# Kernel tuning notes

Measured on AMD Instinct MI355X. Metric: run time of the kernel, lower is better.

## Reference

```python
import jax, jax.numpy as jnp
import numpy as np

B = 4096        # number of (drug, disease) pair graphs
N_PER = 60      # nodes per subgraph (>= k)
N = B * N_PER   # 245760 total nodes
E = 2_000_000   # edges
F_IN = 64
L1, L2 = 32, 32 # latent_dim
K = 30          # sort-pool k
N_DRUG, N_DIS = 1024, 2048


def gcn_conv(x, src, dst, W, b, n):
    # PyG GCNConv (eval): h = XW; symmetric norm with self-loops; out = A_hat h + b
    h = x @ W
    deg = jax.ops.segment_sum(jnp.ones(src.shape[0], h.dtype), dst, num_segments=n) + 1.0
    dinv = deg ** -0.5
    msg = h[src] * (dinv[src] * dinv[dst])[:, None]
    out = jax.ops.segment_sum(msg, dst, num_segments=n)
    out = out + h * (dinv * dinv)[:, None]  # self-loop contribution
    return out + b


def dense_gcn(x, adj, W, b):
    # PyG DenseGCNConv: set diag to 1, D^-1/2 A D^-1/2, out = A_hat (x W) + b
    n = adj.shape[0]
    eye = jnp.eye(n, dtype=adj.dtype)
    a = adj * (1.0 - eye) + eye
    deg = a.sum(-1)
    dinv = jnp.where(deg > 0, deg ** -0.5, 0.0)
    a = dinv[:, None] * a * dinv[None, :]
    return a @ (x @ W) + b


def conv1d(x, w, b, stride):
    out = jax.lax.conv_general_dilated(x, w, (stride,), 'VALID',
                                       dimension_numbers=('NCH', 'OIH', 'NCH'))
    return out + b[None, :, None]


def setup_inputs():
    key = jax.random.key(0)
    ks = jax.random.split(key, 24)
    x = jax.random.normal(ks[0], (N, F_IN), jnp.float32)
    edge_index = jax.random.randint(ks[1], (2, E), 0, N)
    batch = jnp.repeat(jnp.arange(B), N_PER)
    node = jnp.stack([jax.random.randint(ks[2], (B,), 0, N_DRUG),
                      jax.random.randint(ks[3], (B,), 0, N_DIS)], axis=1)
    di_sim = jax.random.normal(ks[4], (N_DRUG, N_DRUG), jnp.float32)
    dr_sim = jax.random.normal(ks[5], (N_DIS, N_DIS), jnp.float32)
    drug_adj = jax.random.uniform(ks[6], (N_DRUG, N_DRUG), jnp.float32)
    dis_adj = jax.random.uniform(ks[7], (N_DIS, N_DIS), jnp.float32)
    p = jnp.array(0.5, jnp.float32)

    def w(k, shape):
        return jax.random.normal(k, shape, jnp.float32) * 0.05

    z = lambda s: jnp.zeros(s, jnp.float32)
    params = dict(
        W1=w(ks[8], (F_IN, L1)), b1=z((L1,)),
        W2=w(ks[9], (L1, L2)), b2=z((L2,)),
        W3=w(ks[10], (256, 64)), b3=z((64,)),
        W4=w(ks[11], (64, 16)), b4=z((16,)),
        lin_di_w=w(ks[12], (N_DRUG, 256)), lin_di_b=z((256,)),
        lin_dr_w=w(ks[13], (N_DIS, 256)), lin_dr_b=z((256,)),
        c1_w=w(ks[14], (128, 1, L1 + L2)), c1_b=z((128,)),
        c2_w=w(ks[15], (256, 128, 5)), c2_b=z((256,)),
        lin1_w=w(ks[16], (2816, 128)), lin1_b=z((128,)),
        lin2_w=w(ks[17], (128, 32)), lin2_b=z((32,)),
        bn_g=jnp.ones((32,), jnp.float32), bn_b=z((32,)),
        fcs_w=w(ks[18], (64, 32)), fcs_b=z((32,)),
        fcs2_w=w(ks[19], (32, 1)), fcs2_b=z((1,)),
    )
    return dict(x=x, edge_index=edge_index, batch=batch, node=node,
                di_sim=di_sim, dr_sim=dr_sim, drug_adj=drug_adj,
                dis_adj=dis_adj, p=p, **params)


def reference(x, edge_index, batch, node, di_sim, dr_sim, drug_adj, dis_adj, p,
              W1, b1, W2, b2, W3, b3, W4, b4,
              lin_di_w, lin_di_b, lin_dr_w, lin_dr_b,
              c1_w, c1_b, c2_w, c2_b, lin1_w, lin1_b, lin2_w, lin2_b,
              bn_g, bn_b, fcs_w, fcs_b, fcs2_w, fcs2_b):
    src, dst = edge_index[0], edge_index[1]
    # two GCN layers over the pair subgraphs
    x1 = jax.nn.relu(gcn_conv(x, src, dst, W1, b1, N))
    x2 = jax.nn.relu(gcn_conv(x1, src, dst, W2, b2, N))
    cs = jnp.concatenate([x1, x2], axis=1)       # [N, 64]
    D = cs.shape[1]
    # sort-pool: equal-size graphs, batch contiguous -> reshape and sort per graph
    xb = cs.reshape(B, N_PER, D)
    order = jnp.argsort(-xb[:, :, -1], axis=-1)  # descending by last channel
    xs = jnp.take_along_axis(xb, order[:, :, None], axis=1)[:, :K]  # [B, K, D]
    h = xs.reshape(B, 1, K * D)
    h = jax.nn.relu(conv1d(h, c1_w, c1_b, D))    # [B, 128, K]
    h = jax.lax.reduce_window(h, -jnp.inf, jax.lax.max, (1, 1, 2), (1, 1, 2), 'VALID')
    h = jax.nn.relu(conv1d(h, c2_w, c2_b, 1))    # [B, 256, 11]
    h = h.reshape(B, -1)                         # [B, 2816]
    h = jax.nn.relu(h @ lin1_w + lin1_b)
    h = h @ lin2_w + lin2_b
    h = jax.nn.relu(h * bn_g + bn_b)             # BatchNorm eval (mean 0, var 1)
    # dense similarity-graph branches (conv3/conv4 weights shared across branches)
    di_e = di_sim @ lin_di_w + lin_di_b
    di_f = jax.nn.relu(dense_gcn(di_e, drug_adj, W3, b3))
    di_o = jax.nn.relu(dense_gcn(di_f, drug_adj, W4, b4))
    di = di_o[node[:, 0]]
    dr_e = dr_sim @ lin_dr_w + lin_dr_b
    dr_f = jax.nn.relu(dense_gcn(dr_e, dis_adj, W3, b3))
    dr_o = jax.nn.relu(dense_gcn(dr_f, dis_adj, W4, b4))
    dr = dr_o[node[:, 1]]
    feat = jnp.concatenate([di, dr], axis=1)     # [B, 32]
    z = jnp.concatenate([h * p, feat * (1.0 - p)], axis=1)  # [B, 64]
    z = jax.nn.relu(z @ fcs_w + fcs_b)
    return (z @ fcs2_w + fcs2_b)[:, 0]
```

## Files before the change

kernel.cpp:

```cpp
#include <hip/hip_runtime.h>

#define NN 245760
#define NB 4096
#define NPER 60
#define NE 2000000
#define KSEL 30
#define NDRUG 1024
#define NDIS 2048
#define NBKT 480
#define CHUNK 8192
#define SEGCAP 4992

typedef unsigned short ushort_t;
typedef unsigned int uint_t;
using bf16x8 = __attribute__((ext_vector_type(8))) short;
using f32x4 = __attribute__((ext_vector_type(4))) float;

__device__ inline ushort_t f2bf(float f) {
    union { float f; unsigned int u; } v; v.f = f;
    unsigned int r = v.u + 0x7FFF + ((v.u >> 16) & 1);
    return (ushort_t)(r >> 16);
}

__global__ void k_bcount(const int* __restrict__ ei, int* __restrict__ bcnt) {
    __shared__ int h[NBKT];
    int t = threadIdx.x;
    for (int i = t; i < NBKT; i += 256) h[i] = 0;
    __syncthreads();
    for (int e = blockIdx.x * 256 + t; e < NE; e += gridDim.x * 256)
        atomicAdd(&h[ei[NE + e] >> 9], 1);
    __syncthreads();
    for (int i = t; i < NBKT; i += 256) if (h[i]) atomicAdd(&bcnt[i], h[i]);
}

__global__ void k_bscan(const int* __restrict__ bcnt, int* __restrict__ bofs) {
    __shared__ int a[512], b_[512];
    int t = threadIdx.x;
    int v = (t < NBKT) ? bcnt[t] : 0;
    a[t] = v; __syncthreads();
    int* src = a; int* dst = b_;
    for (int off = 1; off < 512; off <<= 1) {
        dst[t] = src[t] + ((t >= off) ? src[t - off] : 0);
        __syncthreads();
        int* tmp = src; src = dst; dst = tmp;
    }
    if (t < NBKT) bofs[t] = src[t] - v;
}

__global__ __launch_bounds__(256) void k_bscatter(const int* __restrict__ ei,
                                                  const int* __restrict__ bofs,
                                                  int* __restrict__ bfill,
                                                  uint_t* __restrict__ pairs) {
    __shared__ int hist[NBKT], fill[NBKT], gbase[NBKT];
    int t = threadIdx.x;
    long e0 = (long)blockIdx.x * CHUNK;
    int cnt = (int)min((long)CHUNK, (long)NE - e0);
    for (int i = t; i < NBKT; i += 256) { hist[i] = 0; fill[i] = 0; }
    __syncthreads();
    for (int i = t; i < cnt; i += 256)
        atomicAdd(&hist[ei[NE + e0 + i] >> 9], 1);
    __syncthreads();
    for (int i = t; i < NBKT; i += 256)
        if (hist[i]) gbase[i] = bofs[i] + atomicAdd(&bfill[i], hist[i]);
    __syncthreads();
    for (int i = t; i < cnt; i += 256) {
        int s = ei[e0 + i], d = ei[NE + e0 + i];
        int b = d >> 9;
        int pos = gbase[b] + atomicAdd(&fill[b], 1);
        pairs[pos] = ((uint_t)s << 9) | (uint_t)(d & 511);
    }
}

__global__ __launch_bounds__(256) void k_bbuild(const uint_t* __restrict__ pairs,
                                                const int* __restrict__ bofs,
                                                const int* __restrict__ bcnt,
                                                int* __restrict__ csr,
                                                int* __restrict__ rowp,
                                                int* __restrict__ cntg,
                                                float* __restrict__ dinv) {
    __shared__ int hist[512], nbase[512], nfill[512], scanA[512], scanB[512];
    __shared__ int seg[SEGCAP];
    int t = threadIdx.x, b = blockIdx.x;
    int ebase = bofs[b], ecnt = bcnt[b];
    if (ecnt > SEGCAP) ecnt = SEGCAP;
    for (int i = t; i < 512; i += 256) { hist[i] = 0; nfill[i] = 0; }
    __syncthreads();
    for (int i = t; i < ecnt; i += 256)
        atomicAdd(&hist[pairs[ebase + i] & 511], 1);
    __syncthreads();
    for (int i = t; i < 512; i += 256) scanA[i] = hist[i];
    __syncthreads();
    int* src = scanA; int* dst = scanB;
    for (int off = 1; off < 512; off <<= 1) {
        for (int i = t; i < 512; i += 256)
            dst[i] = src[i] + ((i >= off) ? src[i - off] : 0);
        __syncthreads();
        int* tmp = src; src = dst; dst = tmp;
    }
    for (int i = t; i < 512; i += 256) {
        int h = hist[i];
        int excl = src[i] - h;
        nbase[i] = excl;
        int n = (b << 9) + i;
        rowp[n] = ebase + excl;
        cntg[n] = h;
        dinv[n] = 1.0f / sqrtf((float)h + 1.0f);
    }
    __syncthreads();
    for (int i = t; i < ecnt; i += 256) {
        uint_t v = pairs[ebase + i];
        int ln = v & 511;
        int pos = nbase[ln] + atomicAdd(&nfill[ln], 1);
        if (pos < SEGCAP) seg[pos] = (int)(v >> 9);
    }
    __syncthreads();
    for (int i = t; i < ecnt; i += 256) csr[ebase + i] = seg[i];
}

__global__ __launch_bounds__(256) void k_xw(const float* __restrict__ A, const float* __restrict__ W,
                                            float* __restrict__ h, int K, int lda) {
    __shared__ float Xs[64][65];
    __shared__ float Ws[64][32];
    int t = threadIdx.x;
    int r0 = blockIdx.x * 64;
    int kq = K >> 2;
    for (int idx = t; idx < 64 * kq; idx += 256) {
        int row = idx / kq, q = idx % kq;
        float4 v = *(const float4*)(A + (long)(r0 + row) * lda + q * 4);
        Xs[row][q * 4 + 0] = v.x; Xs[row][q * 4 + 1] = v.y;
        Xs[row][q * 4 + 2] = v.z; Xs[row][q * 4 + 3] = v.w;
    }
    for (int idx = t; idx < K * 32; idx += 256) ((float*)Ws)[idx] = W[idx];
    __syncthreads();
    int r = (t >> 3) * 2, c = (t & 7) * 4;
    float4 acc0 = {0, 0, 0, 0}, acc1 = {0, 0, 0, 0};
    for (int k = 0; k < K; k++) {
        float x0 = Xs[r][k], x1 = Xs[r + 1][k];
        float4 w = *(const float4*)&Ws[k][c];
        acc0.x += x0 * w.x; acc0.y += x0 * w.y; acc0.z += x0 * w.z; acc0.w += x0 * w.w;
        acc1.x += x1 * w.x; acc1.y += x1 * w.y; acc1.z += x1 * w.z; acc1.w += x1 * w.w;
    }
    *(float4*)(h + (long)(r0 + r) * 32 + c) = acc0;
    *(float4*)(h + (long)(r0 + r + 1) * 32 + c) = acc1;
}

__global__ void k_gcn_agg(const float* __restrict__ h, const int* __restrict__ csr,
                          const int* __restrict__ rowp, const int* __restrict__ cnt,
                          const float* __restrict__ dinv, const float* __restrict__ bias,
                          float* __restrict__ out, int colofs) {
    int t = threadIdx.x;
    int l = t & 7, g = t >> 3;
    int wl = t & 63;
    int gbase = wl & ~7;
    int d = blockIdx.x * 32 + g;
    float dd = dinv[d];
    int start = rowp[d], c = cnt[d];
    float4 hv = *(const float4*)(h + (long)d * 32 + l * 4);
    float4 acc; acc.x = dd * hv.x; acc.y = dd * hv.y; acc.z = dd * hv.z; acc.w = dd * hv.w;
    int k = 0;
    while (k < c) {
        int nb = c - k; if (nb > 8) nb = 8;
        int sl = (l < nb) ? csr[start + k + l] : 0;
        int sj[8]; float ds[8]; float4 hj[8];
#pragma unroll
        for (int j = 0; j < 8; j++)
            sj[j] = __shfl(sl, gbase + j, 64);
#pragma unroll
        for (int j = 0; j < 8; j++)
            if (j < nb) ds[j] = dinv[sj[j]];
#pragma unroll
        for (int j = 0; j < 8; j++)
            if (j < nb) hj[j] = *(const float4*)(h + (long)sj[j] * 32 + l * 4);
#pragma unroll
        for (int j = 0; j < 8; j++) {
            if (j < nb) {
                acc.x += ds[j] * hj[j].x;
                acc.y += ds[j] * hj[j].y;
                acc.z += ds[j] * hj[j].z;
                acc.w += ds[j] * hj[j].w;
            }
        }
        k += nb;
    }
    float4 bv = *(const float4*)(bias + l * 4);
    float* op = out + (long)d * 64 + colofs + l * 4;
    op[0] = fmaxf(dd * acc.x + bv.x, 0.f);
    op[1] = fmaxf(dd * acc.y + bv.y, 0.f);
    op[2] = fmaxf(dd * acc.z + bv.z, 0.f);
    op[3] = fmaxf(dd * acc.w + bv.w, 0.f);
}

__global__ __launch_bounds__(256, 2) void k_conv1_mfma(const float* __restrict__ cs,
                                                       const int* __restrict__ sel,
                                                       const ushort_t* __restrict__ c1w16,
                                                       const float* __restrict__ c1b,
                                                       ushort_t* __restrict__ po16) {
    __shared__ ushort_t A_lds[128 * 72];
    __shared__ ushort_t B_lds[128 * 72];
    int t = threadIdx.x;
    int r0 = blockIdx.x * 128;
#pragma unroll
    for (int rnd = 0; rnd < 4; rnd++) {
        int idx = t + rnd * 256;
        int row = idx >> 3, seg = idx & 7;
        const float* src = cs + (long)sel[r0 + row] * 64 + seg * 8;
        float4 v0 = *(const float4*)src;
        float4 v1 = *(const float4*)(src + 4);
        ushort_t tmp[8] = {f2bf(v0.x), f2bf(v0.y), f2bf(v0.z), f2bf(v0.w),
                           f2bf(v1.x), f2bf(v1.y), f2bf(v1.z), f2bf(v1.w)};
        *(uint4*)&A_lds[row * 72 + seg * 8] = *(uint4*)tmp;
        *(uint4*)&B_lds[row * 72 + seg * 8] = *(const uint4*)(c1w16 + row * 64 + seg * 8);
    }
    __syncthreads();
    int wv = t >> 6, lane = t & 63;
    int wm = wv >> 1, wn = wv & 1;
    int lrow = lane & 15, lk = (lane >> 4) * 8, lr4 = (lane >> 4) * 4;
    f32x4 acc[4][4] = {};
#pragma unroll
    for (int kk = 0; kk < 2; kk++) {
        bf16x8 a[4], b[4];
#pragma unroll
        for (int f = 0; f < 4; f++) {
            a[f] = *(const bf16x8*)&A_lds[(wm * 64 + f * 16 + lrow) * 72 + kk * 32 + lk];
            b[f] = *(const bf16x8*)&B_lds[(wn * 64 + f * 16 + lrow) * 72 + kk * 32 + lk];
        }
#pragma unroll
        for (int i = 0; i < 4; i++)
#pragma unroll
            for (int j = 0; j < 4; j++)
                acc[i][j] = __builtin_amdgcn_mfma_f32_16x16x32_bf16(a[i], b[j], acc[i][j], 0, 0, 0);
    }
    __syncthreads();
    ushort_t* po_lds = A_lds;
#pragma unroll
    for (int fn = 0; fn < 4; fn++) {
        int col = wn * 64 + fn * 16 + lrow;
        float bb = c1b[col];
#pragma unroll
        for (int fm = 0; fm < 4; fm++) {
            int lrow2 = wm * 32 + fm * 8 + (lr4 >> 1);
            float v0 = fmaxf(acc[fm][fn][0] + bb, 0.f);
            float v1 = fmaxf(acc[fm][fn][1] + bb, 0.f);
            float v2 = fmaxf(acc[fm][fn][2] + bb, 0.f);
            float v3 = fmaxf(acc[fm][fn][3] + bb, 0.f);
            po_lds[lrow2 * 128 + col]       = f2bf(fmaxf(v0, v1));
            po_lds[(lrow2 + 1) * 128 + col] = f2bf(fmaxf(v2, v3));
        }
    }
    __syncthreads();
    uint4* dst = (uint4*)(po16 + (long)(r0 >> 1) * 128);
    const uint4* srcp = (const uint4*)po_lds;
#pragma unroll
    for (int i = 0; i < 4; i++) dst[t + i * 256] = srcp[t + i * 256];
}

__global__ __launch_bounds__(256, 2) void k_conv2_mfma(const ushort_t* __restrict__ pool16,
                                                       const ushort_t* __restrict__ w2colT,
                                                       ushort_t* __restrict__ act2,
                                                       const float* __restrict__ bias) {
    __shared__ ushort_t smem[2 * 128 * 72];
    ushort_t* A_lds = smem;
    ushort_t* B_lds = smem + 128 * 72;
    int t = threadIdx.x;
    int r0 = blockIdx.x * 128, c0 = blockIdx.y * 128;
    long abase[4]; const ushort_t* bptr[4]; int lofs[4];
#pragma unroll
    for (int rnd = 0; rnd < 4; rnd++) {
        int idx = t + rnd * 256;
        int row = idx >> 3, seg = idx & 7;
        int arow = r0 + row;
        int bb = arow / 11, tt2 = arow - bb * 11;
        abase[rnd] = (long)(bb * 15 + tt2) * 128 + seg * 8;
        bptr[rnd] = w2colT + (long)(c0 + row) * 640 + seg * 8;
        lofs[rnd] = row * 72 + seg * 8;
    }
    int wv = t >> 6, lane = t & 63;
    int wm = wv >> 1, wn = wv & 1;
    int lrow = lane & 15, lk = (lane >> 4) * 8, lr4 = (lane >> 4) * 4;
    f32x4 acc[4][4] = {};
    for (int k0 = 0; k0 < 640; k0 += 64) {
#pragma unroll
        for (int rnd = 0; rnd < 4; rnd++) {
            *(uint4*)&A_lds[lofs[rnd]] = *(const uint4*)(pool16 + abase[rnd] + k0);
            *(uint4*)&B_lds[lofs[rnd]] = *(const uint4*)(bptr[rnd] + k0);
        }
        __syncthreads();
#pragma unroll
        for (int kk = 0; kk < 2; kk++) {
            bf16x8 a[4], b[4];
#pragma unroll
            for (int f = 0; f < 4; f++) {
                a[f] = *(const bf16x8*)&A_lds[(wm * 64 + f * 16 + lrow) * 72 + kk * 32 + lk];
                b[f] = *(const bf16x8*)&B_lds[(wn * 64 + f * 16 + lrow) * 72 + kk * 32 + lk];
            }
#pragma unroll
            for (int i = 0; i < 4; i++)
#pragma unroll
                for (int j = 0; j < 4; j++)
                    acc[i][j] = __builtin_amdgcn_mfma_f32_16x16x32_bf16(a[i], b[j], acc[i][j], 0, 0, 0);
        }
        __syncthreads();
    }
    ushort_t* c_lds = smem;
#pragma unroll
    for (int fn = 0; fn < 4; fn++) {
        int col = wn * 64 + fn * 16 + lrow;
        float bv = bias[c0 + col];
#pragma unroll
        for (int fm = 0; fm < 4; fm++) {
            int lr = wm * 64 + fm * 16 + lr4;
#pragma unroll
            for (int j = 0; j < 4; j++)
                c_lds[(lr + j) * 128 + col] = f2bf(fmaxf(acc[fm][fn][j] + bv, 0.f));
        }
    }
    __syncthreads();
#pragma unroll
    for (int i = 0; i < 8; i++) {
        int idx = t + i * 256;
        int row = idx >> 4, q = idx & 15;
        *(uint4*)(act2 + (long)(r0 + row) * 256 + c0 + q * 8) = ((const uint4*)c_lds)[idx];
    }
}

__global__ __launch_bounds__(256, 2) void k_lin1_mfma(const ushort_t* __restrict__ A,
                                                      const ushort_t* __restrict__ Bm,
                                                      float* __restrict__ C) {
    __shared__ ushort_t A_lds[128 * 72];
    __shared__ ushort_t B_lds[128 * 72];
    int t = threadIdx.x;
    int r0 = blockIdx.x * 128;
    int kz = blockIdx.z;
    const ushort_t* ap[4]; const ushort_t* bp[4]; int lofs[4];
#pragma unroll
    for (int rnd = 0; rnd < 4; rnd++) {
        int idx = t + rnd * 256;
        int row = idx >> 3, seg = idx & 7;
        ap[rnd] = A + (long)(r0 + row) * 2816 + kz * 704 + seg * 8;
        bp[rnd] = Bm + (long)row * 2816 + kz * 704 + seg * 8;
        lofs[rnd] = row * 72 + seg * 8;
    }
    int wv = t >> 6, lane = t & 63;
    int wm = wv >> 1, wn = wv & 1;
    int lrow = lane & 15, lk = (lane >> 4) * 8, lr4 = (lane >> 4) * 4;
    f32x4 acc[4][4] = {};
    for (int k0 = 0; k0 < 704; k0 += 64) {
#pragma unroll
        for (int rnd = 0; rnd < 4; rnd++) {
            *(uint4*)&A_lds[lofs[rnd]] = *(const uint4*)(ap[rnd] + k0);
            *(uint4*)&B_lds[lofs[rnd]] = *(const uint4*)(bp[rnd] + k0);
        }
        __syncthreads();
#pragma unroll
        for (int kk = 0; kk < 2; kk++) {
            bf16x8 a[4], b[4];
#pragma unroll
            for (int f = 0; f < 4; f++) {
                a[f] = *(const bf16x8*)&A_lds[(wm * 64 + f * 16 + lrow) * 72 + kk * 32 + lk];
                b[f] = *(const bf16x8*)&B_lds[(wn * 64 + f * 16 + lrow) * 72 + kk * 32 + lk];
            }
#pragma unroll
            for (int i = 0; i < 4; i++)
#pragma unroll
                for (int j = 0; j < 4; j++)
                    acc[i][j] = __builtin_amdgcn_mfma_f32_16x16x32_bf16(a[i], b[j], acc[i][j], 0, 0, 0);
        }
        __syncthreads();
    }
#pragma unroll
    for (int fn = 0; fn < 4; fn++) {
        int col = wn * 64 + fn * 16 + lrow;
#pragma unroll
        for (int fm = 0; fm < 4; fm++) {
            int rowb = r0 + wm * 64 + fm * 16 + lr4;
#pragma unroll
            for (int j = 0; j < 4; j++)
                atomicAdd(&C[(long)(rowb + j) * 128 + col], acc[fm][fn][j]);
        }
    }
}

__global__ __launch_bounds__(256, 2) void k_de_mfma(
    const ushort_t* __restrict__ A0, const ushort_t* __restrict__ B0, float* __restrict__ C0,
    const float* __restrict__ bias0, int M0, int K0, int KS0,
    const ushort_t* __restrict__ A1, const ushort_t* __restrict__ B1, float* __restrict__ C1,
    const float* __restrict__ bias1, int M1, int K1, int KS1) {
    __shared__ ushort_t A_lds[128 * 72];
    __shared__ ushort_t B_lds[64 * 72];
    int z = blockIdx.z;
    const ushort_t* A; const ushort_t* Bm; float* C; const float* bias; int M, K, kz, KS;
    if (z < KS0) { A = A0; Bm = B0; C = C0; bias = bias0; M = M0; K = K0; kz = z; KS = KS0; }
    else { A = A1; Bm = B1; C = C1; bias = bias1; M = M1; K = K1; kz = z - KS0; KS = KS1; }
    int r0 = blockIdx.x * 128, c0 = blockIdx.y * 64;
    if (r0 >= M) return;
    int Kc = K / KS;
    int kb = kz * Kc;
    int t = threadIdx.x;
    const ushort_t* ap[4]; int alofs[4];
#pragma unroll
    for (int rnd = 0; rnd < 4; rnd++) {
        int idx = t + rnd * 256;
        int row = idx >> 3, seg = idx & 7;
        ap[rnd] = A + (long)(r0 + row) * K + kb + seg * 8;
        alofs[rnd] = row * 72 + seg * 8;
    }
    const ushort_t* bp[2]; int blofs[2];
#pragma unroll
    for (int rnd = 0; rnd < 2; rnd++) {
        int idx = t + rnd * 256;
        int row = idx >> 3, seg = idx & 7;
        bp[rnd] = Bm + (long)(c0 + row) * K + kb + seg * 8;
        blofs[rnd] = row * 72 + seg * 8;
    }
    int wv = t >> 6, lane = t & 63;
    int lrow = lane & 15, lk = (lane >> 4) * 8, lr4 = (lane >> 4) * 4;
    uint4 areg[4], breg[2];
#pragma unroll
    for (int rnd = 0; rnd < 4; rnd++) areg[rnd] = *(const uint4*)(ap[rnd]);
#pragma unroll
    for (int rnd = 0; rnd < 2; rnd++) breg[rnd] = *(const uint4*)(bp[rnd]);
    f32x4 acc[2][4] = {};
    for (int k0 = 0; k0 < Kc; k0 += 64) {
#pragma unroll
        for (int rnd = 0; rnd < 4; rnd++) *(uint4*)&A_lds[alofs[rnd]] = areg[rnd];
#pragma unroll
        for (int rnd = 0; rnd < 2; rnd++) *(uint4*)&B_lds[blofs[rnd]] = breg[rnd];
        __syncthreads();
        if (k0 + 64 < Kc) {
#pragma unroll
            for (int rnd = 0; rnd < 4; rnd++) areg[rnd] = *(const uint4*)(ap[rnd] + k0 + 64);
#pragma unroll
            for (int rnd = 0; rnd < 2; rnd++) breg[rnd] = *(const uint4*)(bp[rnd] + k0 + 64);
        }
#pragma unroll
        for (int kk = 0; kk < 2; kk++) {
            bf16x8 a[2], b[4];
#pragma unroll
            for (int f = 0; f < 2; f++)
                a[f] = *(const bf16x8*)&A_lds[(wv * 32 + f * 16 + lrow) * 72 + kk * 32 + lk];
#pragma unroll
            for (int f = 0; f < 4; f++)
                b[f] = *(const bf16x8*)&B_lds[(f * 16 + lrow) * 72 + kk * 32 + lk];
#pragma unroll
            for (int i = 0; i < 2; i++)
#pragma unroll
                for (int j = 0; j < 4; j++)
                    acc[i][j] = __builtin_amdgcn_mfma_f32_16x16x32_bf16(a[i], b[j], acc[i][j], 0, 0, 0);
        }
        __syncthreads();
    }
#pragma unroll
    for (int fn = 0; fn < 4; fn++) {
        int col = c0 + fn * 16 + lrow;
        float bv = (kz == 0) ? bias[col] : 0.f;
#pragma unroll
        for (int fm = 0; fm < 2; fm++) {
            int rowb = r0 + wv * 32 + fm * 16 + lr4;
#pragma unroll
            for (int j = 0; j < 4; j++)
                atomicAdd(&C[(long)(rowb + j) * 256 + col], acc[fm][fn][j] + bv);
        }
    }
}

__global__ __launch_bounds__(256, 2) void k_g_mfma(
    const ushort_t* __restrict__ A0, const ushort_t* __restrict__ B0, float* __restrict__ C0,
    int M0, int K0, int KS0,
    const ushort_t* __restrict__ A1, const ushort_t* __restrict__ B1, float* __restrict__ C1,
    int M1, int K1, int KS1) {
    __shared__ ushort_t A_lds[128 * 72];
    __shared__ ushort_t B_lds[64 * 72];
    int z = blockIdx.z;
    const ushort_t* A; const ushort_t* Bm; float* C; int M, K, kz, KS;
    if (z < KS0) { A = A0; Bm = B0; C = C0; M = M0; K = K0; kz = z; KS = KS0; }
    else { A = A1; Bm = B1; C = C1; M = M1; K = K1; kz = z - KS0; KS = KS1; }
    int r0 = blockIdx.x * 128;
    if (r0 >= M) return;
    int Kc = K / KS;
    int kb = kz * Kc;
    int t = threadIdx.x;
    const ushort_t* ap[4]; int alofs[4];
#pragma unroll
    for (int rnd = 0; rnd < 4; rnd++) {
        int idx = t + rnd * 256;
        int row = idx >> 3, seg = idx & 7;
        ap[rnd] = A + (long)(r0 + row) * K + kb + seg * 8;
        alofs[rnd] = row * 72 + seg * 8;
    }
    const ushort_t* bp[2]; int blofs[2];
#pragma unroll
    for (int rnd = 0; rnd < 2; rnd++) {
        int idx = t + rnd * 256;
        int row = idx >> 3, seg = idx & 7;
        bp[rnd] = Bm + (long)row * K + kb + seg * 8;
        blofs[rnd] = row * 72 + seg * 8;
    }
    int wv = t >> 6, lane = t & 63;
    int lrow = lane & 15, lk = (lane >> 4) * 8, lr4 = (lane >> 4) * 4;
    uint4 areg[4], breg[2];
#pragma unroll
    for (int rnd = 0; rnd < 4; rnd++) areg[rnd] = *(const uint4*)(ap[rnd]);
#pragma unroll
    for (int rnd = 0; rnd < 2; rnd++) breg[rnd] = *(const uint4*)(bp[rnd]);
    f32x4 acc[2][4] = {};
    for (int k0 = 0; k0 < Kc; k0 += 64) {
#pragma unroll
        for (int rnd = 0; rnd < 4; rnd++) *(uint4*)&A_lds[alofs[rnd]] = areg[rnd];
#pragma unroll
        for (int rnd = 0; rnd < 2; rnd++) *(uint4*)&B_lds[blofs[rnd]] = breg[rnd];
        __syncthreads();
        if (k0 + 64 < Kc) {
#pragma unroll
            for (int rnd = 0; rnd < 4; rnd++) areg[rnd] = *(const uint4*)(ap[rnd] + k0 + 64);
#pragma unroll
            for (int rnd = 0; rnd < 2; rnd++) breg[rnd] = *(const uint4*)(bp[rnd] + k0 + 64);
        }
#pragma unroll
        for (int kk = 0; kk < 2; kk++) {
            bf16x8 a[2], b[4];
#pragma unroll
            for (int f = 0; f < 2; f++)
                a[f] = *(const bf16x8*)&A_lds[(wv * 32 + f * 16 + lrow) * 72 + kk * 32 + lk];
#pragma unroll
            for (int f = 0; f < 4; f++)
                b[f] = *(const bf16x8*)&B_lds[(f * 16 + lrow) * 72 + kk * 32 + lk];
#pragma unroll
            for (int i = 0; i < 2; i++)
#pragma unroll
                for (int j = 0; j < 4; j++)
                    acc[i][j] = __builtin_amdgcn_mfma_f32_16x16x32_bf16(a[i], b[j], acc[i][j], 0, 0, 0);
        }
        __syncthreads();
    }
#pragma unroll
    for (int fn = 0; fn < 4; fn++) {
        int col = fn * 16 + lrow;
#pragma unroll
        for (int fm = 0; fm < 2; fm++) {
            int rowb = r0 + wv * 32 + fm * 16 + lr4;
#pragma unroll
            for (int j = 0; j < 4; j++)
                atomicAdd(&C[(long)(rowb + j) * 64 + col], acc[fm][fn][j]);
        }
    }
}

__global__ void k_cvt2(const float* __restrict__ a0, ushort_t* __restrict__ o0, long n0,
                       const float* __restrict__ a1, ushort_t* __restrict__ o1, long n1) {
    long i4 = ((long)blockIdx.x * 256 + threadIdx.x) * 4;
    const float* a; ushort_t* o;
    if (i4 < n0) { a = a0 + i4; o = o0 + i4; }
    else {
        long j = i4 - n0;
        if (j >= n1) return;
        a = a1 + j; o = o1 + j;
    }
    float4 v = *(const float4*)a;
    o[0] = f2bf(v.x); o[1] = f2bf(v.y); o[2] = f2bf(v.z); o[3] = f2bf(v.w);
}

__global__ void k_linwT2(const float* __restrict__ w0, ushort_t* __restrict__ o0, int K0,
                         const float* __restrict__ w1, ushort_t* __restrict__ o1, int K1) {
    __shared__ float tile[64][65];
    int nb0 = K0 / 64;
    int bx = blockIdx.x;
    const float* w; ushort_t* o; int K, kt;
    if (bx < nb0) { w = w0; o = o0; K = K0; kt = bx; }
    else { w = w1; o = o1; K = K1; kt = bx - nb0; }
    int n0 = blockIdx.y * 64, k0 = kt * 64;
    int t = threadIdx.x;
    int r = t >> 6, c = t & 63;
    for (int rr = r; rr < 64; rr += 4)
        tile[rr][c] = w[(long)(k0 + rr) * 256 + n0 + c];
    __syncthreads();
    for (int rr = r; rr < 64; rr += 4)
        o[(long)(n0 + rr) * K + k0 + c] = f2bf(tile[c][rr]);
}

__global__ void k_uT2(const float* __restrict__ u0, ushort_t* __restrict__ o0, int K0,
                      const float* __restrict__ u1, ushort_t* __restrict__ o1, int K1) {
    __shared__ float tile[64][65];
    int nb0 = K0 / 64;
    int bx = blockIdx.x;
    const float* u; ushort_t* o; int K, kt;
    if (bx < nb0) { u = u0; o = o0; K = K0; kt = bx; }
    else { u = u1; o = o1; K = K1; kt = bx - nb0; }
    int k0 = kt * 64;
    int t = threadIdx.x;
    int r = t >> 6, c = t & 63;
    for (int rr = r; rr < 64; rr += 4)
        tile[rr][c] = u[(long)(k0 + rr) * 64 + c];
    __syncthreads();
    for (int rr = r; rr < 64; rr += 4)
        o[(long)rr * K + k0 + c] = f2bf(tile[c][rr]);
}

__global__ __launch_bounds__(256) void k_gemm_sk(
    const float* A0, const float* B0, float* C0, const float* ab0p, const float* cs0p,
    int M0, int N0, int K0, int lda0, int KS0, int Kc0,
    const float* A1, const float* B1, float* C1, const float* ab1p, const float* cs1p,
    int M1, int N1, int K1, int lda1, int KS1, int Kc1) {
    int z = blockIdx.z;
    const float* A; const float* Bm; float* C; const float* abp; const float* csp;
    int M, N, K, lda, kz, Kc;
    if (z < KS0) { A = A0; Bm = B0; C = C0; abp = ab0p; csp = cs0p; M = M0; N = N0; K = K0; lda = lda0; kz = z; Kc = Kc0; }
    else { A = A1; Bm = B1; C = C1; abp = ab1p; csp = cs1p; M = M1; N = N1; K = K1; lda = lda1; kz = z - KS0; Kc = Kc1; }
    int r0 = blockIdx.x * 64, c0 = blockIdx.y * 64;
    if (r0 >= M || c0 >= N) return;
    int kb = kz * Kc, ke = min(K, kb + Kc);
    __shared__ float As[16][68];
    __shared__ float Bs[16][68];
    int t = threadIdx.x;
    int tx = t & 15, ty = t >> 4;
    float acc[4][4] = {};
    int ar = t >> 2, aq = (t & 3) * 4;
    long abase = (long)(r0 + ar) * lda;
    int brow = t >> 4, bc = (t & 15) * 4;
    float4 av = *(const float4*)(A + abase + kb + aq);
    if (abp) {
        float4 abv = *(const float4*)(abp + kb + aq);
        av.x += abv.x; av.y += abv.y; av.z += abv.z; av.w += abv.w;
    }
    float4 bv = *(const float4*)(Bm + (long)(kb + brow) * N + c0 + bc);
    for (int k0 = kb; k0 < ke; k0 += 16) {
        As[aq + 0][ar] = av.x; As[aq + 1][ar] = av.y; As[aq + 2][ar] = av.z; As[aq + 3][ar] = av.w;
        *(float4*)&Bs[brow][bc] = bv;
        __syncthreads();
        if (k0 + 16 < ke) {
            av = *(const float4*)(A + abase + k0 + 16 + aq);
            if (abp) {
                float4 abv = *(const float4*)(abp + k0 + 16 + aq);
                av.x += abv.x; av.y += abv.y; av.z += abv.z; av.w += abv.w;
            }
            bv = *(const float4*)(Bm + (long)(k0 + 16 + brow) * N + c0 + bc);
        }
#pragma unroll
        for (int kk = 0; kk < 16; kk++) {
            float4 a4 = *(const float4*)&As[kk][ty * 4];
            float4 b4 = *(const float4*)&Bs[kk][tx * 4];
            float aa[4] = {a4.x, a4.y, a4.z, a4.w};
            float bb2[4] = {b4.x, b4.y, b4.z, b4.w};
#pragma unroll
            for (int i = 0; i < 4; i++)
#pragma unroll
                for (int j = 0; j < 4; j++) acc[i][j] += aa[i] * bb2[j];
        }
        __syncthreads();
    }
#pragma unroll
    for (int i = 0; i < 4; i++) {
        int row = r0 + ty * 4 + i;
        float sc = csp ? csp[row] : 1.0f;
#pragma unroll
        for (int j = 0; j < 4; j++)
            atomicAdd(&C[(long)row * N + c0 + tx * 4 + j], acc[i][j] * sc);
    }
}

__global__ void k_dense_deg2(const float* __restrict__ adj0, float* __restrict__ d0, int n0,
                             const float* __restrict__ adj1, float* __restrict__ d1, int n1) {
    int lane = threadIdx.x & 63;
    int row = (blockIdx.x * blockDim.x + threadIdx.x) >> 6;
    const float* adj; float* dv; int n, r;
    if (row < n0) { adj = adj0; dv = d0; n = n0; r = row; }
    else {
        r = row - n0;
        if (r >= n1) return;
        adj = adj1; dv = d1; n = n1;
    }
    const float* rp = adj + (long)r * n;
    float s = 0.f;
    for (int j = lane; j < n; j += 64) s += rp[j];
    for (int off = 32; off > 0; off >>= 1) s += __shfl_down(s, off, 64);
    if (lane == 0) {
        float deg = s - rp[r] + 1.0f;
        dv[r] = (deg > 0.f) ? 1.0f / sqrtf(deg) : 0.f;
    }
}

__global__ void k_fix_w4(const float* g0, const float* u0, const float* adj0, const float* d0, float* o0, int n0,
                         const float* g1, const float* u1, const float* adj1, const float* d1, float* o1, int n1,
                         const float* __restrict__ b3, const float* __restrict__ W4) {
    __shared__ float dfs[16][68];
    __shared__ float W4s[64 * 16];
    int t = threadIdx.x;
    for (int i = t; i < 1024; i += 256) W4s[i] = W4[i];
    int bx = blockIdx.x, nb0 = n0 / 16;
    const float* g; const float* u; const float* adj; const float* dv; float* o; int n, r0;
    if (bx < nb0) { g = g0; u = u0; adj = adj0; dv = d0; o = o0; n = n0; r0 = bx * 16; }
    else { g = g1; u = u1; adj = adj1; dv = d1; o = o1; n = n1; r0 = (bx - nb0) * 16; }
    int r = t >> 4;
    int row = r0 + r;
    float di = dv[row];
    float om = 1.0f - adj[(long)row * n + row];
    int c4 = (t & 15) * 4;
    float4 gv = *(const float4*)(g + (long)row * 64 + c4);
    float4 uv = *(const float4*)(u + (long)row * 64 + c4);
    float4 bv = *(const float4*)(b3 + c4);
    dfs[r][c4 + 0] = fmaxf(di * (gv.x + om * uv.x) + bv.x, 0.f);
    dfs[r][c4 + 1] = fmaxf(di * (gv.y + om * uv.y) + bv.y, 0.f);
    dfs[r][c4 + 2] = fmaxf(di * (gv.z + om * uv.z) + bv.z, 0.f);
    dfs[r][c4 + 3] = fmaxf(di * (gv.w + om * uv.w) + bv.w, 0.f);
    __syncthreads();
    int c = t & 15;
    float accv = 0.f;
#pragma unroll
    for (int k = 0; k < 64; k++) accv += dfs[r][k] * W4s[k * 16 + c];
    o[row * 16 + c] = di * accv;
}

__global__ void k_fixup2(const float* g0, const float* t0, const float* adj0, const float* d0, float* C0, long n0,
                         const float* g1, const float* t1, const float* adj1, const float* d1, float* C1, long n1,
                         const float* bias, int cols) {
    long idx = (long)blockIdx.x * 256 + threadIdx.x;
    long s0 = n0 * cols;
    const float* g; const float* tt; const float* adj; const float* dv; float* C; long n, li;
    if (idx < s0) { g = g0; tt = t0; adj = adj0; dv = d0; C = C0; n = n0; li = idx; }
    else {
        li = idx - s0;
        if (li >= n1 * cols) return;
        g = g1; tt = t1; adj = adj1; dv = d1; C = C1; n = n1;
    }
    long i = li / cols; int j = li % cols;
    float v = dv[i] * (g[li] + (1.0f - adj[i * n + i]) * tt[li]) + bias[j];
    C[li] = fmaxf(v, 0.f);
}

__global__ void k_adj16(const float* adj0, const float* u0, float* C0, int n0, int KS0, int Kc0,
                        const float* adj1, const float* u1, float* C1, int n1, int KS1, int Kc1) {
    int z = blockIdx.z;
    const float* adj; const float* u; float* C; int n, kz, Kc;
    if (z < KS0) { adj = adj0; u = u0; C = C0; n = n0; kz = z; Kc = Kc0; }
    else { adj = adj1; u = u1; C = C1; n = n1; kz = z - KS0; Kc = Kc1; }
    int r0 = blockIdx.x * 16;
    if (r0 >= n) return;
    int t = threadIdx.x;
    int r = r0 + (t >> 4), c = t & 15;
    int kb = kz * Kc, ke = min(n, kb + Kc);
    const float* arp = adj + (long)r * n;
    float acc = 0.f;
    for (int k = kb; k < ke; k += 4) {
        float4 a = *(const float4*)(arp + k);
        acc += a.x * u[(k + 0) * 16 + c] + a.y * u[(k + 1) * 16 + c]
             + a.z * u[(k + 2) * 16 + c] + a.w * u[(k + 3) * 16 + c];
    }
    atomicAdd(&C[r * 16 + c], acc);
}

__global__ void k_select(const float* __restrict__ cs, int* __restrict__ sel) {
    __shared__ float kk[240];
    int t = threadIdx.x;
    int b0 = blockIdx.x * 4;
    if (t < 240) kk[t] = cs[((long)(b0 * 60 + t)) * 64 + 63];
    __syncthreads();
    if (t < 240) {
        int lb = t / 60, i = t % 60;
        float key = kk[lb * 60 + i];
        int r = 0;
        for (int j = 0; j < 60; j++) {
            float kj = kk[lb * 60 + j];
            r += (kj > key) || (kj == key && j < i);
        }
        if (r < KSEL) sel[(b0 + lb) * KSEL + r] = (b0 + lb) * 60 + i;
    }
}

__global__ void k_w2colT(const float* __restrict__ c2w, ushort_t* __restrict__ o) {
    int idx = blockIdx.x * blockDim.x + threadIdx.x;
    if (idx >= 256 * 640) return;
    int oc = idx / 640, q = idx % 640;
    int tap = q >> 7, ic = q & 127;
    o[idx] = f2bf(c2w[(oc * 128 + ic) * 5 + tap]);
}

__global__ void k_w1pT(const float* __restrict__ w, ushort_t* __restrict__ o) {
    int idx = blockIdx.x * blockDim.x + threadIdx.x;
    if (idx >= 128 * 2816) return;
    int j = idx / 2816, c = idx % 2816;
    int tt = c >> 8, oc = c & 255;
    o[idx] = f2bf(w[(oc * 11 + tt) * 128 + j]);
}

__global__ void k_lin2_bn(const float* __restrict__ x, const float* __restrict__ l1b,
                          const float* __restrict__ w,
                          const float* __restrict__ b, const float* __restrict__ g,
                          const float* __restrict__ bb, float* __restrict__ o) {
    int t = blockIdx.x * blockDim.x + threadIdx.x;
    int j = t & 31, bi = t >> 5;
    const float* xr = x + (long)bi * 128;
    float acc = b[j];
    for (int k = 0; k < 128; k++) acc += fmaxf(xr[k] + l1b[k], 0.f) * w[k * 32 + j];
    o[bi * 32 + j] = fmaxf(acc * g[j] + bb[j], 0.f);
}

__global__ __launch_bounds__(256) void k_final(const float* __restrict__ hfin, const int* __restrict__ node,
                                               const float* __restrict__ dio, const float* __restrict__ dro,
                                               const float* __restrict__ pp,
                                               const float* __restrict__ fw, const float* __restrict__ fb,
                                               const float* __restrict__ f2w, const float* __restrict__ f2b,
                                               float* __restrict__ out) {
    __shared__ float w[64 * 32];
    __shared__ float w2[32];
    int t = threadIdx.x;
    for (int f = t; f < 2048; f += 256) w[f] = fw[f];
    if (t < 32) w2[t] = f2w[t];
    __syncthreads();
    int b = blockIdx.x * 256 + t;
    float p = *pp, q = 1.0f - p;
    float zin[64];
#pragma unroll
    for (int i = 0; i < 32; i++) zin[i] = hfin[b * 32 + i] * p;
    int n0 = node[b * 2], n1 = node[b * 2 + 1];
#pragma unroll
    for (int i = 0; i < 16; i++) zin[32 + i] = dio[n0 * 16 + i] * q;
#pragma unroll
    for (int i = 0; i < 16; i++) zin[48 + i] = dro[n1 * 16 + i] * q;
    float res = f2b[0];
    for (int j = 0; j < 32; j++) {
        float acc = fb[j];
#pragma unroll
        for (int i = 0; i < 64; i++) acc += zin[i] * w[i * 32 + j];
        res += fmaxf(acc, 0.f) * w2[j];
    }
    out[b] = res;
}

extern "C" void kernel_launch(void* const* d_in, const int* in_sizes, int n_in,
                              void* d_out, int out_size, void* d_ws, size_t ws_size,
                              hipStream_t stream) {
    const float* x        = (const float*)d_in[0];
    const int*   ei       = (const int*)d_in[1];
    const int*   node     = (const int*)d_in[3];
    const float* di_sim   = (const float*)d_in[4];
    const float* dr_sim   = (const float*)d_in[5];
    const float* drug_adj = (const float*)d_in[6];
    const float* dis_adj  = (const float*)d_in[7];
    const float* p        = (const float*)d_in[8];
    const float* W1 = (const float*)d_in[9],  *b1 = (const float*)d_in[10];
    const float* W2 = (const float*)d_in[11], *b2 = (const float*)d_in[12];
    const float* W3 = (const float*)d_in[13], *b3 = (const float*)d_in[14];
    const float* W4 = (const float*)d_in[15], *b4 = (const float*)d_in[16];
    const float* lin_di_w = (const float*)d_in[17], *lin_di_b = (const float*)d_in[18];
    const float* lin_dr_w = (const float*)d_in[19], *lin_dr_b = (const float*)d_in[20];
    const float* c1w = (const float*)d_in[21], *c1b = (const float*)d_in[22];
    const float* c2w = (const float*)d_in[23], *c2b = (const float*)d_in[24];
    const float* lin1w = (const float*)d_in[25], *lin1b = (const float*)d_in[26];
    const float* lin2w = (const float*)d_in[27], *lin2b = (const float*)d_in[28];
    const float* bng = (const float*)d_in[29], *bnb = (const float*)d_in[30];
    const float* fcsw = (const float*)d_in[31], *fcsb = (const float*)d_in[32];
    const float* fcs2w = (const float*)d_in[33], *fcs2b = (const float*)d_in[34];

    char* ws = (char*)d_ws;
    size_t o = 0;
    auto alloc = [&](size_t bytes) { size_t r = o; o += (bytes + 255) & ~(size_t)255; return r; };
    int*   csr     = (int*)(ws + alloc((size_t)NE * 4));
    int*   rowp    = (int*)(ws + alloc((size_t)NN * 4));
    int*   degcnt  = (int*)(ws + alloc((size_t)NN * 4));
    float* dinvn   = (float*)(ws + alloc((size_t)NN * 4));
    float* hbuf    = (float*)(ws + alloc((size_t)NN * 32 * 4));
    float* cs      = (float*)(ws + alloc((size_t)NN * 64 * 4));
    int*   sel     = (int*)(ws + alloc((size_t)NB * KSEL * 4));
    float* hfin    = (float*)(ws + alloc((size_t)NB * 32 * 4));
    ushort_t* w2colT = (ushort_t*)(ws + alloc((size_t)256 * 640 * 2));
    ushort_t* w1pT   = (ushort_t*)(ws + alloc((size_t)128 * 2816 * 2));
    int*   bofs    = (int*)(ws + alloc((size_t)NBKT * 4));
    float* ddin_di = (float*)(ws + alloc((size_t)NDRUG * 4));
    float* ddin_dr = (float*)(ws + alloc((size_t)NDIS * 4));
    float* dt2_di  = (float*)(ws + alloc((size_t)NDRUG * 16 * 4));
    float* dt2_dr  = (float*)(ws + alloc((size_t)NDIS * 16 * 4));
    float* do_di   = (float*)(ws + alloc((size_t)NDRUG * 16 * 4));
    float* do_dr   = (float*)(ws + alloc((size_t)NDIS * 16 * 4));
    size_t zbase = o;
    int*   bcnt    = (int*)(ws + alloc((size_t)NBKT * 4));
    int*   bfill   = (int*)(ws + alloc((size_t)NBKT * 4));
    float* lin1o   = (float*)(ws + alloc((size_t)NB * 128 * 4));
    float* de_di   = (float*)(ws + alloc((size_t)NDRUG * 256 * 4));
    float* de_dr   = (float*)(ws + alloc((size_t)NDIS * 256 * 4));
    float* dt_di   = (float*)(ws + alloc((size_t)NDRUG * 64 * 4));
    float* dt_dr   = (float*)(ws + alloc((size_t)NDIS * 64 * 4));
    float* dg_di   = (float*)(ws + alloc((size_t)NDRUG * 64 * 4));
    float* dg_dr   = (float*)(ws + alloc((size_t)NDIS * 64 * 4));
    float* dg2_di  = (float*)(ws + alloc((size_t)NDRUG * 16 * 4));
    float* dg2_dr  = (float*)(ws + alloc((size_t)NDIS * 16 * 4));
    size_t zsize = o - zbase;
    uint_t* pairsg   = (uint_t*)cs;
    ushort_t* pool16 = (ushort_t*)hbuf;
    ushort_t* act2   = (ushort_t*)cs;
    char* hb = (char*)hbuf;
    ushort_t* di_sim16 = (ushort_t*)(hb + 15728640);
    ushort_t* dr_sim16 = (ushort_t*)(hb + 17825792);
    ushort_t* lindiT16 = (ushort_t*)(hb + 26214400);
    ushort_t* lindrT16 = (ushort_t*)(hb + 26738688);
    ushort_t* c1w16    = (ushort_t*)(hb + 27787264);
    ushort_t* uT16_di  = (ushort_t*)(hb + 27811840);
    ushort_t* uT16_dr  = (ushort_t*)(hb + 27942912);
    ushort_t* drugadj16 = di_sim16;
    ushort_t* disadj16  = dr_sim16;

    hipMemsetAsync(ws + zbase, 0, zsize, stream);

    k_bcount<<<512, 256, 0, stream>>>(ei, bcnt);
    k_bscan<<<1, 512, 0, stream>>>(bcnt, bofs);
    k_bscatter<<<(NE + CHUNK - 1) / CHUNK, 256, 0, stream>>>(ei, bofs, bfill, pairsg);
    k_bbuild<<<NBKT, 256, 0, stream>>>(pairsg, bofs, bcnt, csr, rowp, degcnt, dinvn);

    k_xw<<<NN / 64, 256, 0, stream>>>(x, W1, hbuf, 64, 64);
    k_gcn_agg<<<NN / 32, 256, 0, stream>>>(hbuf, csr, rowp, degcnt, dinvn, b1, cs, 0);
    k_xw<<<NN / 64, 256, 0, stream>>>(cs, W2, hbuf, 32, 64);
    k_gcn_agg<<<NN / 32, 256, 0, stream>>>(hbuf, csr, rowp, degcnt, dinvn, b2, cs, 32);

    k_select<<<NB / 4, 256, 0, stream>>>(cs, sel);

    k_cvt2<<<5120, 256, 0, stream>>>(di_sim, di_sim16, (long)NDRUG * NDRUG,
                                     dr_sim, dr_sim16, (long)NDIS * NDIS);
    k_linwT2<<<dim3(48, 4), 256, 0, stream>>>(lin_di_w, lindiT16, NDRUG,
                                              lin_dr_w, lindrT16, NDIS);
    k_de_mfma<<<dim3(16, 4, 12), 256, 0, stream>>>(
        di_sim16, lindiT16, de_di, lin_di_b, NDRUG, NDRUG, 4,
        dr_sim16, lindrT16, de_dr, lin_dr_b, NDIS, NDIS, 8);
    k_dense_deg2<<<(NDRUG + NDIS) * 64 / 256, 256, 0, stream>>>(drug_adj, ddin_di, NDRUG, dis_adj, ddin_dr, NDIS);
    k_cvt2<<<5120, 256, 0, stream>>>(drug_adj, drugadj16, (long)NDRUG * NDRUG,
                                     dis_adj, disadj16, (long)NDIS * NDIS);

    k_cvt2<<<8, 256, 0, stream>>>(c1w, c1w16, 8192, c1w, c1w16, 0);
    k_w2colT<<<(256 * 640 + 255) / 256, 256, 0, stream>>>(c2w, w2colT);
    k_w1pT<<<(128 * 2816 + 255) / 256, 256, 0, stream>>>(lin1w, w1pT);

    k_conv1_mfma<<<960, 256, 0, stream>>>(cs, sel, c1w16, c1b, pool16);

    k_conv2_mfma<<<dim3(352, 2), 256, 0, stream>>>(pool16, w2colT, act2, c2b);

    k_lin1_mfma<<<dim3(32, 1, 4), 256, 0, stream>>>(act2, w1pT, lin1o);
    k_lin2_bn<<<NB * 32 / 256, 256, 0, stream>>>(lin1o, lin1b, lin2w, lin2b, bng, bnb, hfin);

    k_gemm_sk<<<dim3(NDIS / 64, 1, 8), 256, 0, stream>>>(
        de_di, W3, dt_di, nullptr, ddin_di, NDRUG, 64, 256, 256, 4, 64,
        de_dr, W3, dt_dr, nullptr, ddin_dr, NDIS, 64, 256, 256, 4, 64);
    k_uT2<<<48, 256, 0, stream>>>(dt_di, uT16_di, NDRUG, dt_dr, uT16_dr, NDIS);
    k_g_mfma<<<dim3(16, 1, 24), 256, 0, stream>>>(
        drugadj16, uT16_di, dg_di, NDRUG, NDRUG, 8,
        disadj16, uT16_dr, dg_dr, NDIS, NDIS, 16);
    k_fix_w4<<<(NDRUG + NDIS) / 16, 256, 0, stream>>>(
        dg_di, dt_di, drug_adj, ddin_di, dt2_di, NDRUG,
        dg_dr, dt_dr, dis_adj, ddin_dr, dt2_dr, NDIS, b3, W4);
    k_adj16<<<dim3(NDIS / 16, 1, 6), 256, 0, stream>>>(
        drug_adj, dt2_di, dg2_di, NDRUG, 2, 512,
        dis_adj, dt2_dr, dg2_dr, NDIS, 4, 512);
    k_fixup2<<<((NDRUG + NDIS) * 16 + 255) / 256, 256, 0, stream>>>(
        dg2_di, dt2_di, drug_adj, ddin_di, do_di, NDRUG,
        dg2_dr, dt2_dr, dis_adj, ddin_dr, do_dr, NDIS, b4, 16);

    k_final<<<NB / 256, 256, 0, stream>>>(hfin, node, do_di, do_dr, p, fcsw, fcsb, fcs2w, fcs2b, (float*)d_out);
}
```

Before: 458.8 us.

## Use fixed-capacity bucket segments and register-prefetch GEMM tiles

Drops the bucket count and scan kernels by giving each destination bucket a fixed SEGCAP-sized slot in the pairs buffer and CSR array, and clamps writes that overflow the slot. This removes two launches and a full pass over the destination indices. It also double-buffers global loads into registers in the two bf16 MFMA GEMMs, so the next K tile is fetched while the current one is computed. The fixed capacity silently drops edges if a bucket exceeds SEGCAP, a limit the old code already applied in the build step, and the register prefetch raises register pressure.

Result: slower. 529.1 us (+15.3%).

```diff
diff --git a/kernel.cpp b/kernel.cpp
--- a/kernel.cpp
+++ b/kernel.cpp
@@ -22,33 +22,7 @@
     return (ushort_t)(r >> 16);
 }
 
-__global__ void k_bcount(const int* __restrict__ ei, int* __restrict__ bcnt) {
-    __shared__ int h[NBKT];
-    int t = threadIdx.x;
-    for (int i = t; i < NBKT; i += 256) h[i] = 0;
-    __syncthreads();
-    for (int e = blockIdx.x * 256 + t; e < NE; e += gridDim.x * 256)
-        atomicAdd(&h[ei[NE + e] >> 9], 1);
-    __syncthreads();
-    for (int i = t; i < NBKT; i += 256) if (h[i]) atomicAdd(&bcnt[i], h[i]);
-}
-
-__global__ void k_bscan(const int* __restrict__ bcnt, int* __restrict__ bofs) {
-    __shared__ int a[512], b_[512];
-    int t = threadIdx.x;
-    int v = (t < NBKT) ? bcnt[t] : 0;
-    a[t] = v; __syncthreads();
-    int* src = a; int* dst = b_;
-    for (int off = 1; off < 512; off <<= 1) {
-        dst[t] = src[t] + ((t >= off) ? src[t - off] : 0);
-        __syncthreads();
-        int* tmp = src; src = dst; dst = tmp;
-    }
-    if (t < NBKT) bofs[t] = src[t] - v;
-}
-
 __global__ __launch_bounds__(256) void k_bscatter(const int* __restrict__ ei,
-                                                  const int* __restrict__ bofs,
                                                   int* __restrict__ bfill,
                                                   uint_t* __restrict__ pairs) {
     __shared__ int hist[NBKT], fill[NBKT], gbase[NBKT];
@@ -61,19 +35,19 @@
         atomicAdd(&hist[ei[NE + e0 + i] >> 9], 1);
     __syncthreads();
     for (int i = t; i < NBKT; i += 256)
-        if (hist[i]) gbase[i] = bofs[i] + atomicAdd(&bfill[i], hist[i]);
+        if (hist[i]) gbase[i] = i * SEGCAP + atomicAdd(&bfill[i], hist[i]);
     __syncthreads();
     for (int i = t; i < cnt; i += 256) {
         int s = ei[e0 + i], d = ei[NE + e0 + i];
         int b = d >> 9;
         int pos = gbase[b] + atomicAdd(&fill[b], 1);
-        pairs[pos] = ((uint_t)s << 9) | (uint_t)(d & 511);
+        if (pos < (b + 1) * SEGCAP)
+            pairs[pos] = ((uint_t)s << 9) | (uint_t)(d & 511);
     }
 }
 
 __global__ __launch_bounds__(256) void k_bbuild(const uint_t* __restrict__ pairs,
-                                                const int* __restrict__ bofs,
-                                                const int* __restrict__ bcnt,
+                                                const int* __restrict__ bfill,
                                                 int* __restrict__ csr,
                                                 int* __restrict__ rowp,
                                                 int* __restrict__ cntg,
@@ -81,7 +55,8 @@
     __shared__ int hist[512], nbase[512], nfill[512], scanA[512], scanB[512];
     __shared__ int seg[SEGCAP];
     int t = threadIdx.x, b = blockIdx.x;
-    int ebase = bofs[b], ecnt = bcnt[b];
+    int ebase = b * SEGCAP;
+    int ecnt = bfill[b];
     if (ecnt > SEGCAP) ecnt = SEGCAP;
     for (int i = t; i < 512; i += 256) { hist[i] = 0; nfill[i] = 0; }
     __syncthreads();
@@ -277,14 +252,27 @@
     int wv = t >> 6, lane = t & 63;
     int wm = wv >> 1, wn = wv & 1;
     int lrow = lane & 15, lk = (lane >> 4) * 8, lr4 = (lane >> 4) * 4;
+    uint4 areg[4], breg[4];
+#pragma unroll
+    for (int rnd = 0; rnd < 4; rnd++) {
+        areg[rnd] = *(const uint4*)(pool16 + abase[rnd]);
+        breg[rnd] = *(const uint4*)(bptr[rnd]);
+    }
     f32x4 acc[4][4] = {};
     for (int k0 = 0; k0 < 640; k0 += 64) {
 #pragma unroll
         for (int rnd = 0; rnd < 4; rnd++) {
-            *(uint4*)&A_lds[lofs[rnd]] = *(const uint4*)(pool16 + abase[rnd] + k0);
-            *(uint4*)&B_lds[lofs[rnd]] = *(const uint4*)(bptr[rnd] + k0);
-        }
-        __syncthreads();
+            *(uint4*)&A_lds[lofs[rnd]] = areg[rnd];
+            *(uint4*)&B_lds[lofs[rnd]] = breg[rnd];
+        }
+        __syncthreads();
+        if (k0 + 64 < 640) {
+#pragma unroll
+            for (int rnd = 0; rnd < 4; rnd++) {
+                areg[rnd] = *(const uint4*)(pool16 + abase[rnd] + k0 + 64);
+                breg[rnd] = *(const uint4*)(bptr[rnd] + k0 + 64);
+            }
+        }
 #pragma unroll
         for (int kk = 0; kk < 2; kk++) {
             bf16x8 a[4], b[4];
@@ -343,14 +331,27 @@
     int wv = t >> 6, lane = t & 63;
     int wm = wv >> 1, wn = wv & 1;
     int lrow = lane & 15, lk = (lane >> 4) * 8, lr4 = (lane >> 4) * 4;
+    uint4 areg[4], breg[4];
+#pragma unroll
+    for (int rnd = 0; rnd < 4; rnd++) {
+        areg[rnd] = *(const uint4*)(ap[rnd]);
+        breg[rnd] = *(const uint4*)(bp[rnd]);
+    }
     f32x4 acc[4][4] = {};
     for (int k0 = 0; k0 < 704; k0 += 64) {
 #pragma unroll
         for (int rnd = 0; rnd < 4; rnd++) {
-            *(uint4*)&A_lds[lofs[rnd]] = *(const uint4*)(ap[rnd] + k0);
-            *(uint4*)&B_lds[lofs[rnd]] = *(const uint4*)(bp[rnd] + k0);
-        }
-        __syncthreads();
+            *(uint4*)&A_lds[lofs[rnd]] = areg[rnd];
+            *(uint4*)&B_lds[lofs[rnd]] = breg[rnd];
+        }
+        __syncthreads();
+        if (k0 + 64 < 704) {
+#pragma unroll
+            for (int rnd = 0; rnd < 4; rnd++) {
+                areg[rnd] = *(const uint4*)(ap[rnd] + k0 + 64);
+                breg[rnd] = *(const uint4*)(bp[rnd] + k0 + 64);
+            }
+        }
 #pragma unroll
         for (int kk = 0; kk < 2; kk++) {
             bf16x8 a[4], b[4];
@@ -853,7 +854,7 @@
     char* ws = (char*)d_ws;
     size_t o = 0;
     auto alloc = [&](size_t bytes) { size_t r = o; o += (bytes + 255) & ~(size_t)255; return r; };
-    int*   csr     = (int*)(ws + alloc((size_t)NE * 4));
+    int*   csr     = (int*)(ws + alloc((size_t)NBKT * SEGCAP * 4));
     int*   rowp    = (int*)(ws + alloc((size_t)NN * 4));
     int*   degcnt  = (int*)(ws + alloc((size_t)NN * 4));
     float* dinvn   = (float*)(ws + alloc((size_t)NN * 4));
@@ -863,7 +864,6 @@
     float* hfin    = (float*)(ws + alloc((size_t)NB * 32 * 4));
     ushort_t* w2colT = (ushort_t*)(ws + alloc((size_t)256 * 640 * 2));
     ushort_t* w1pT   = (ushort_t*)(ws + alloc((size_t)128 * 2816 * 2));
-    int*   bofs    = (int*)(ws + alloc((size_t)NBKT * 4));
     float* ddin_di = (float*)(ws + alloc((size_t)NDRUG * 4));
     float* ddin_dr = (float*)(ws + alloc((size_t)NDIS * 4));
     float* dt2_di  = (float*)(ws + alloc((size_t)NDRUG * 16 * 4));
@@ -871,7 +871,6 @@
     float* do_di   = (float*)(ws + alloc((size_t)NDRUG * 16 * 4));
     float* do_dr   = (float*)(ws + alloc((size_t)NDIS * 16 * 4));
     size_t zbase = o;
-    int*   bcnt    = (int*)(ws + alloc((size_t)NBKT * 4));
     int*   bfill   = (int*)(ws + alloc((size_t)NBKT * 4));
     float* lin1o   = (float*)(ws + alloc((size_t)NB * 128 * 4));
     float* de_di   = (float*)(ws + alloc((size_t)NDRUG * 256 * 4));
@@ -899,10 +898,8 @@
 
     hipMemsetAsync(ws + zbase, 0, zsize, stream);
 
-    k_bcount<<<512, 256, 0, stream>>>(ei, bcnt);
-    k_bscan<<<1, 512, 0, stream>>>(bcnt, bofs);
-    k_bscatter<<<(NE + CHUNK - 1) / CHUNK, 256, 0, stream>>>(ei, bofs, bfill, pairsg);
-    k_bbuild<<<NBKT, 256, 0, stream>>>(pairsg, bofs, bcnt, csr, rowp, degcnt, dinvn);
+    k_bscatter<<<(NE + CHUNK - 1) / CHUNK, 256, 0, stream>>>(ei, bfill, pairsg);
+    k_bbuild<<<NBKT, 256, 0, stream>>>(pairsg, bfill, csr, rowp, degcnt, dinvn);
 
     k_xw<<<NN / 64, 256, 0, stream>>>(x, W1, hbuf, 64, 64);
     k_gcn_agg<<<NN / 32, 256, 0, stream>>>(hbuf, csr, rowp, degcnt, dinvn, b1, cs, 0);
```
